# Optimization experiments

Measured on AMD Instinct MI355X. Metric: run time of the kernel, lower is better.

## Reference

```python
import jax, jax.numpy as jnp
import numpy as np

BATCH, K, N, D = 8192, 8, 1024, 256
BETA = 0.25


def setup_inputs() -> dict:
    key = jax.random.key(0)
    kx, ke = jax.random.split(key)
    x = jax.random.normal(kx, (BATCH, K, D), dtype=jnp.float32)
    entries = jax.random.normal(ke, (K, N, D), dtype=jnp.float32)
    return {"x": x, "entries": entries}


def reference(x, entries):
    # x: [b, k, d]; entries: [k, n, d]
    xt = jnp.transpose(x, (1, 0, 2))  # [k, b, d]
    # squared euclidean distances (argmin is identical to cdist argmin)
    d2 = (
        jnp.sum(xt * xt, axis=-1)[:, :, None]
        + jnp.sum(entries * entries, axis=-1)[:, None, :]
        - 2.0 * jnp.einsum("kbd,knd->kbn", xt, entries)
    )  # [k, b, n]
    idx = jnp.argmin(d2, axis=-1)  # [k, b]
    quantized = jnp.take_along_axis(entries, idx[:, :, None], axis=1)  # [k, b, d]
    quantized = jnp.transpose(quantized, (1, 0, 2))  # [b, k, d]
    # straight-through estimator
    x_q = x + jax.lax.stop_gradient(quantized - x)
    dictionary_loss = jnp.mean(
        jnp.sum((jax.lax.stop_gradient(x) - quantized) ** 2, axis=-1)
    )
    commitment_loss = BETA * jnp.mean(
        jnp.sum((x - jax.lax.stop_gradient(quantized)) ** 2, axis=-1)
    )
    return x_q, jnp.transpose(idx, (1, 0)), dictionary_loss, commitment_loss
```

## Files before the change

### kernel.cpp

```cpp
#include <hip/hip_runtime.h>
#include <cstdint>
#include <cstddef>

#define BATCH 8192
#define KC 8
#define NC 1024
#define DC 256
#define TAU 1e-3f

typedef __attribute__((ext_vector_type(8))) _Float16 half8;
typedef __attribute__((ext_vector_type(4))) _Float16 half4;
typedef __attribute__((ext_vector_type(4))) float floatx4;

__device__ __forceinline__ void async_load16(const void* g, void* l) {
    __builtin_amdgcn_global_load_lds((const __attribute__((address_space(1))) uint32_t*)g,
                                     (__attribute__((address_space(3))) uint32_t*)l, 16, 0, 0);
}
__device__ __forceinline__ unsigned sortable(float v) {
    unsigned u = __float_as_uint(v);
    return u ^ (unsigned)(((int)u >> 31) | 0x80000000);
}
__device__ __forceinline__ float unsortable(unsigned ks) {
    unsigned u = (ks & 0x80000000u) ? (ks ^ 0x80000000u) : ~ks;
    return __uint_as_float(u);
}
__device__ __forceinline__ unsigned long long umin64(unsigned long long a, unsigned long long b) { return a < b ? a : b; }
__device__ __forceinline__ unsigned long long umax64(unsigned long long a, unsigned long long b) { return a > b ? a : b; }

__device__ __forceinline__ int lidx(int r, int c) {
    return (r >> 3) * 1024 + (r & 7) * 128 + ((c ^ (r & 7)) * 16);
}
__device__ __forceinline__ half8 ldsr(const char* base, int r, int c) {
    return *(const half8*)(base + lidx(r, c));
}

__global__ __launch_bounds__(256) void prep_e_kernel(const float* __restrict__ entries,
                                                     _Float16* __restrict__ Ecat,
                                                     float* __restrict__ eef) {
    int wave = threadIdx.x >> 6, lane = threadIdx.x & 63;
    int row = blockIdx.x * 4 + wave;
    float4 v = ((const float4*)(entries + (size_t)row * DC))[lane];
    half4 h, l;
    h.x = (_Float16)v.x; h.y = (_Float16)v.y; h.z = (_Float16)v.z; h.w = (_Float16)v.w;
    l.x = (_Float16)(v.x - (float)h.x); l.y = (_Float16)(v.y - (float)h.y);
    l.z = (_Float16)(v.z - (float)h.z); l.w = (_Float16)(v.w - (float)h.w);
    _Float16* rp = Ecat + (size_t)row * 512;
    *(half4*)(rp + lane * 4)       = h;
    *(half4*)(rp + 256 + lane * 4) = l;
    double s = (double)v.x * v.x + (double)v.y * v.y + (double)v.z * v.z + (double)v.w * v.w;
    #pragma unroll
    for (int off = 32; off > 0; off >>= 1) s += __shfl_down(s, off, 64);
    if (lane == 0) eef[row] = (float)s;
}

__global__ __launch_bounds__(256, 2) void vq_gemm(const float* __restrict__ x,
                                                  const float* __restrict__ entries,
                                                  const _Float16* __restrict__ Ecat,
                                                  const float* __restrict__ eef,
                                                  float* __restrict__ out_idx,
                                                  float* __restrict__ out_q,
                                                  double* __restrict__ partial,
                                                  int* __restrict__ flag_list,
                                                  int* __restrict__ flag_cnt) {
    __shared__ alignas(16) char Bh[2][16384];
    __shared__ alignas(16) char Bl[2][16384];
    __shared__ float eef_lds[NC];
    __shared__ unsigned long long top2a[128], top2b[128];
    __shared__ int idx_lds[128];
    __shared__ double red[256];

    const int t = threadIdx.x;
    const int k  = blockIdx.x & 7;
    const int b0 = (blockIdx.x >> 3) * 128;
    const int w = t >> 6, lane = t & 63;
    const int quad = lane >> 4, col = lane & 15;
    const int rl = lane >> 3;
    const int cs = (lane & 7) ^ rl;

    { float4 v = ((const float4*)(eef + (size_t)k * NC))[t]; *(float4*)(eef_lds + t * 4) = v; }
    if (t < 128) { top2a[t] = ~0ull; top2b[t] = ~0ull; }

    half8 Ah[2][8], Al[2][8];
    #pragma unroll
    for (int mi = 0; mi < 2; ++mi) {
        const float* xrow = x + ((size_t)(b0 + w * 32 + mi * 16 + col) * KC + k) * DC + quad * 8;
        #pragma unroll
        for (int ks = 0; ks < 8; ++ks) {
            float4 u0 = *(const float4*)(xrow + ks * 32);
            float4 u1 = *(const float4*)(xrow + ks * 32 + 4);
            float f[8] = {u0.x, u0.y, u0.z, u0.w, u1.x, u1.y, u1.z, u1.w};
            half8 h, l;
            #pragma unroll
            for (int j = 0; j < 8; ++j) {
                h[j] = (_Float16)f[j];
                l[j] = (_Float16)(f[j] - (float)h[j]);
            }
            Ah[mi][ks] = h; Al[mi][ks] = l;
        }
    }

    const char* EcatK = (const char*)(Ecat + (size_t)k * NC * 512);
    #define ISSUE_B(buf, n0b, dcb)                                                          \
        {                                                                                   \
            _Pragma("unroll")                                                               \
            for (int j = 0; j < 8; ++j) {                                                   \
                int li = w * 8 + j; int tile = li >> 4, grp = li & 15;                      \
                const char* src = EcatK + (size_t)((n0b) + grp * 8 + rl) * 1024             \
                                + tile * 512 + (dcb) * 2 + cs * 16;                         \
                char* dst = (tile ? Bl[buf] : Bh[buf]) + grp * 1024 + lane * 16;            \
                async_load16(src, dst);                                                     \
            }                                                                               \
        }

    ISSUE_B(0, 0, 0);

    for (int nt = 0; nt < 8; ++nt) {
        const int n0 = nt * 128;
        floatx4 acc[2][8] = {};
        #pragma unroll
        for (int dcs = 0; dcs < 4; ++dcs) {
            const int step = nt * 4 + dcs;
            __syncthreads();
            if (step < 31) {
                const int ns = step + 1;
                ISSUE_B(ns & 1, (ns >> 2) * 128, (ns & 3) * 64);
            }
            const int cur = step & 1;
            #pragma unroll
            for (int kk = 0; kk < 2; ++kk) {
                const int cb = kk * 4 + quad;
                const int ks = dcs * 2 + kk;
                #pragma unroll
                for (int ni = 0; ni < 8; ++ni) {
                    half8 bh = ldsr(Bh[cur], ni * 16 + col, cb);
                    acc[0][ni] = __builtin_amdgcn_mfma_f32_16x16x32_f16(Ah[0][ks], bh, acc[0][ni], 0, 0, 0);
                    acc[1][ni] = __builtin_amdgcn_mfma_f32_16x16x32_f16(Ah[1][ks], bh, acc[1][ni], 0, 0, 0);
                    acc[0][ni] = __builtin_amdgcn_mfma_f32_16x16x32_f16(Al[0][ks], bh, acc[0][ni], 0, 0, 0);
                    acc[1][ni] = __builtin_amdgcn_mfma_f32_16x16x32_f16(Al[1][ks], bh, acc[1][ni], 0, 0, 0);
                    half8 bl = ldsr(Bl[cur], ni * 16 + col, cb);
                    acc[0][ni] = __builtin_amdgcn_mfma_f32_16x16x32_f16(Ah[0][ks], bl, acc[0][ni], 0, 0, 0);
                    acc[1][ni] = __builtin_amdgcn_mfma_f32_16x16x32_f16(Ah[1][ks], bl, acc[1][ni], 0, 0, 0);
                }
            }
        }
        float ev[8];
        #pragma unroll
        for (int ni = 0; ni < 8; ++ni) ev[ni] = eef_lds[n0 + ni * 16 + col];
        #pragma unroll
        for (int mi = 0; mi < 2; ++mi) {
            #pragma unroll
            for (int reg = 0; reg < 4; ++reg) {
                unsigned long long a1 = ~0ull, a2 = ~0ull;
                #pragma unroll
                for (int ni = 0; ni < 8; ++ni) {
                    float val = fmaf(-2.0f, acc[mi][ni][reg], ev[ni]);
                    unsigned long long key = (((unsigned long long)sortable(val)) << 32)
                                           | (unsigned)(n0 + ni * 16 + col);
                    bool lt1 = key < a1, lt2 = key < a2;
                    a2 = lt1 ? a1 : (lt2 ? key : a2);
                    a1 = lt1 ? key : a1;
                }
                #pragma unroll
                for (int off = 1; off < 16; off <<= 1) {
                    unsigned long long o1 = __shfl_xor(a1, off, 16);
                    unsigned long long o2 = __shfl_xor(a2, off, 16);
                    unsigned long long m1 = umin64(a1, o1);
                    unsigned long long m2 = umin64(umax64(a1, o1), umin64(a2, o2));
                    a1 = m1; a2 = m2;
                }
                if (col == 0) {
                    int row = w * 32 + mi * 16 + quad * 4 + reg;
                    unsigned long long t1 = top2a[row], t2 = top2b[row];
                    top2a[row] = umin64(t1, a1);
                    top2b[row] = umin64(umax64(t1, a1), umin64(t2, a2));
                }
            }
        }
    }

    __syncthreads();
    if (t < 128) {
        unsigned long long a1 = top2a[t], a2 = top2b[t];
        float v1 = unsortable((unsigned)(a1 >> 32));
        float v2 = unsortable((unsigned)(a2 >> 32));
        int rid = (b0 + t) * KC + k;
        if (v2 - v1 < TAU) {
            int pos = atomicAdd(flag_cnt, 1);
            flag_list[pos] = rid;
            idx_lds[t] = -1;
        } else {
            int n = (int)(unsigned)(a1 & 0xFFFFFFFFull);
            idx_lds[t] = n;
            out_idx[rid] = (float)n;
        }
    }
    __syncthreads();

    double s = 0.0;
    #pragma unroll
    for (int rr = 0; rr < 8; ++rr) {
        int r = rr * 16 + (t >> 4);
        int c = t & 15;
        int n = idx_lds[r];
        if (n >= 0) {
            const float4* xp = (const float4*)(x + ((size_t)(b0 + r) * KC + k) * DC);
            const float4* ep = (const float4*)(entries + ((size_t)k * NC + n) * DC);
            float4* op = (float4*)(out_q + ((size_t)(b0 + r) * KC + k) * DC);
            #pragma unroll
            for (int j = 0; j < 4; ++j) {
                int ci = j * 16 + c;
                float4 xv = xp[ci], evv = ep[ci];
                op[ci] = evv;
                double d0 = (double)xv.x - evv.x, d1 = (double)xv.y - evv.y;
                double d2 = (double)xv.z - evv.z, d3 = (double)xv.w - evv.w;
                s += d0 * d0 + d1 * d1 + d2 * d2 + d3 * d3;
            }
        }
    }
    red[t] = s;
    __syncthreads();
    for (int off2 = 128; off2 > 0; off2 >>= 1) {
        if (t < off2) red[t] += red[t + off2];
        __syncthreads();
    }
    if (t == 0) partial[blockIdx.x] = red[0];
    #undef ISSUE_B
}

__global__ __launch_bounds__(256) void refine_kernel(const float* __restrict__ x,
                                                     const float* __restrict__ entries,
                                                     const int* __restrict__ flag_list,
                                                     const int* __restrict__ flag_cnt,
                                                     float* __restrict__ out_idx,
                                                     float* __restrict__ out_q,
                                                     double* __restrict__ refAcc) {
    __shared__ float xs[DC];
    __shared__ double bd[256];
    __shared__ int    bi[256];
    __shared__ int    win;
    const int t = threadIdx.x;
    int cnt = *flag_cnt;
    for (int i = blockIdx.x; i < cnt; i += gridDim.x) {
        int rid = flag_list[i];
        int k = rid & 7;
        __syncthreads();
        xs[t] = x[(size_t)rid * DC + t];
        __syncthreads();
        double best = 1.0e300; int bn = 0;
        for (int e = 0; e < 4; ++e) {
            int n = t * 4 + e;
            const float* ep = entries + ((size_t)k * NC + n) * DC;
            double s = 0.0;
            for (int d = 0; d < DC; ++d) {
                double df = (double)xs[d] - (double)ep[d];
                s += df * df;
            }
            if (s < best) { best = s; bn = n; }
        }
        bd[t] = best; bi[t] = bn;
        __syncthreads();
        for (int s2 = 128; s2 > 0; s2 >>= 1) {
            if (t < s2) {
                if (bd[t + s2] < bd[t] || (bd[t + s2] == bd[t] && bi[t + s2] < bi[t])) {
                    bd[t] = bd[t + s2]; bi[t] = bi[t + s2];
                }
            }
            __syncthreads();
        }
        if (t == 0) {
            out_idx[rid] = (float)bi[0];
            win = bi[0];
            atomicAdd(refAcc, bd[0]);
        }
        __syncthreads();
        out_q[(size_t)rid * DC + t] = entries[((size_t)k * NC + win) * DC + t];
    }
}

__global__ __launch_bounds__(256) void finalize_kernel(const double* __restrict__ partial,
                                                       const double* __restrict__ refAcc,
                                                       float* __restrict__ out) {
    __shared__ double red[256];
    const int t = threadIdx.x;
    double s = 0.0;
    for (int i = t; i < 512; i += 256) s += partial[i];
    red[t] = s;
    __syncthreads();
    for (int off = 128; off > 0; off >>= 1) {
        if (t < off) red[t] += red[t + off];
        __syncthreads();
    }
    if (t == 0) {
        double L = (red[0] + *refAcc) * (1.0 / 65536.0);
        out[(size_t)BATCH * KC * DC + BATCH * KC + 0] = (float)L;
        out[(size_t)BATCH * KC * DC + BATCH * KC + 1] = (float)(0.25 * L);
    }
}

extern "C" void kernel_launch(void* const* d_in, const int* in_sizes, int n_in,
                              void* d_out, int out_size, void* d_ws, size_t ws_size,
                              hipStream_t stream) {
    const float* x       = (const float*)d_in[0];
    const float* entries = (const float*)d_in[1];
    float* out = (float*)d_out;

    char* ws = (char*)d_ws;
    int*      flag_cnt  = (int*)ws;
    double*   refAcc    = (double*)(ws + 8);
    double*   partial   = (double*)(ws + 4096);
    float*    eef       = (float*)(ws + 65536);
    int*      flag_list = (int*)(ws + 131072);
    _Float16* Ecat      = (_Float16*)(ws + 1048576);

    float* out_q   = out;
    float* out_idx = out + (size_t)BATCH * KC * DC;

    hipMemsetAsync(ws, 0, 16, stream);
    prep_e_kernel<<<KC * NC / 4, 256, 0, stream>>>(entries, Ecat, eef);
    vq_gemm<<<512, 256, 0, stream>>>(x, entries, Ecat, eef, out_idx, out_q,
                                     partial, flag_list, flag_cnt);
    refine_kernel<<<128, 256, 0, stream>>>(x, entries, flag_list, flag_cnt,
                                           out_idx, out_q, refAcc);
    finalize_kernel<<<1, 256, 0, stream>>>(partial, refAcc, out);
}
```

Baseline: 274.8 us.

## Use float top-2 argmin tracking and wave-parallel refine distance computation

Replaces the packed 64-bit sortable key top-2 tracking in the GEMM epilogue with separate float values and an int index, cutting 64-bit compares and shuffles in the argmin reduction. Separately, the refine kernel now assigns one codebook entry per wave iteration with lanes splitting the dimension, giving coalesced float4 loads and shuffle reductions. Previously each thread looped serially over 256 dimensions with strided loads. Tie-breaking on equal distances may now favour a different index within the GEMM epilogue, which the refine fallback only partly covers.

After: 372.7 us. +35.6%, slower.

```diff
diff --git a/kernel.cpp b/kernel.cpp
--- a/kernel.cpp
+++ b/kernel.cpp
@@ -16,16 +16,6 @@
     __builtin_amdgcn_global_load_lds((const __attribute__((address_space(1))) uint32_t*)g,
                                      (__attribute__((address_space(3))) uint32_t*)l, 16, 0, 0);
 }
-__device__ __forceinline__ unsigned sortable(float v) {
-    unsigned u = __float_as_uint(v);
-    return u ^ (unsigned)(((int)u >> 31) | 0x80000000);
-}
-__device__ __forceinline__ float unsortable(unsigned ks) {
-    unsigned u = (ks & 0x80000000u) ? (ks ^ 0x80000000u) : ~ks;
-    return __uint_as_float(u);
-}
-__device__ __forceinline__ unsigned long long umin64(unsigned long long a, unsigned long long b) { return a < b ? a : b; }
-__device__ __forceinline__ unsigned long long umax64(unsigned long long a, unsigned long long b) { return a > b ? a : b; }
 
 __device__ __forceinline__ int lidx(int r, int c) {
     return (r >> 3) * 1024 + (r & 7) * 128 + ((c ^ (r & 7)) * 16);
@@ -65,7 +55,9 @@
     __shared__ alignas(16) char Bh[2][16384];
     __shared__ alignas(16) char Bl[2][16384];
     __shared__ float eef_lds[NC];
-    __shared__ unsigned long long top2a[128], top2b[128];
+    __shared__ float tv1[128];
+    __shared__ float tv2[128];
+    __shared__ int   ti1[128];
     __shared__ int idx_lds[128];
     __shared__ double red[256];
 
@@ -78,7 +70,7 @@
     const int cs = (lane & 7) ^ rl;
 
     { float4 v = ((const float4*)(eef + (size_t)k * NC))[t]; *(float4*)(eef_lds + t * 4) = v; }
-    if (t < 128) { top2a[t] = ~0ull; top2b[t] = ~0ull; }
+    if (t < 128) { tv1[t] = 1e30f; tv2[t] = 1e30f; ti1[t] = 0; }
 
     half8 Ah[2][8], Al[2][8];
     #pragma unroll
@@ -150,29 +142,37 @@
         for (int mi = 0; mi < 2; ++mi) {
             #pragma unroll
             for (int reg = 0; reg < 4; ++reg) {
-                unsigned long long a1 = ~0ull, a2 = ~0ull;
+                float v1 = 1e30f, v2 = 1e30f; int i1 = 0;
                 #pragma unroll
                 for (int ni = 0; ni < 8; ++ni) {
                     float val = fmaf(-2.0f, acc[mi][ni][reg], ev[ni]);
-                    unsigned long long key = (((unsigned long long)sortable(val)) << 32)
-                                           | (unsigned)(n0 + ni * 16 + col);
-                    bool lt1 = key < a1, lt2 = key < a2;
-                    a2 = lt1 ? a1 : (lt2 ? key : a2);
-                    a1 = lt1 ? key : a1;
+                    int n = n0 + ni * 16 + col;
+                    bool lt1 = val < v1;
+                    bool lt2 = val < v2;
+                    float nv2 = lt1 ? v1 : (lt2 ? val : v2);
+                    v1 = lt1 ? val : v1;
+                    i1 = lt1 ? n : i1;
+                    v2 = nv2;
                 }
                 #pragma unroll
                 for (int off = 1; off < 16; off <<= 1) {
-                    unsigned long long o1 = __shfl_xor(a1, off, 16);
-                    unsigned long long o2 = __shfl_xor(a2, off, 16);
-                    unsigned long long m1 = umin64(a1, o1);
-                    unsigned long long m2 = umin64(umax64(a1, o1), umin64(a2, o2));
-                    a1 = m1; a2 = m2;
+                    float o1 = __shfl_xor(v1, off, 16);
+                    float o2 = __shfl_xor(v2, off, 16);
+                    int   oi = __shfl_xor(i1, off, 16);
+                    bool sw = o1 < v1;
+                    float hi = sw ? v1 : o1;
+                    v1 = sw ? o1 : v1;
+                    i1 = sw ? oi : i1;
+                    v2 = fminf(fminf(v2, o2), hi);
                 }
                 if (col == 0) {
                     int row = w * 32 + mi * 16 + quad * 4 + reg;
-                    unsigned long long t1 = top2a[row], t2 = top2b[row];
-                    top2a[row] = umin64(t1, a1);
-                    top2b[row] = umin64(umax64(t1, a1), umin64(t2, a2));
+                    float t1 = tv1[row], t2 = tv2[row];
+                    bool sw = v1 < t1;
+                    float hi = sw ? t1 : v1;
+                    tv2[row] = fminf(fminf(t2, v2), hi);
+                    tv1[row] = sw ? v1 : t1;
+                    if (sw) ti1[row] = i1;
                 }
             }
         }
@@ -180,16 +180,14 @@
 
     __syncthreads();
     if (t < 128) {
-        unsigned long long a1 = top2a[t], a2 = top2b[t];
-        float v1 = unsortable((unsigned)(a1 >> 32));
-        float v2 = unsortable((unsigned)(a2 >> 32));
+        float v1 = tv1[t], v2 = tv2[t];
         int rid = (b0 + t) * KC + k;
         if (v2 - v1 < TAU) {
             int pos = atomicAdd(flag_cnt, 1);
             flag_list[pos] = rid;
             idx_lds[t] = -1;
         } else {
-            int n = (int)(unsigned)(a1 & 0xFFFFFFFFull);
+            int n = ti1[t];
             idx_lds[t] = n;
             out_idx[rid] = (float)n;
         }
@@ -234,46 +232,44 @@
                                                      float* __restrict__ out_idx,
                                                      float* __restrict__ out_q,
                                                      double* __restrict__ refAcc) {
-    __shared__ float xs[DC];
-    __shared__ double bd[256];
-    __shared__ int    bi[256];
+    __shared__ double wbest[4];
+    __shared__ int    wbn[4];
     __shared__ int    win;
     const int t = threadIdx.x;
+    const int wave = t >> 6, lane = t & 63;
     int cnt = *flag_cnt;
     for (int i = blockIdx.x; i < cnt; i += gridDim.x) {
         int rid = flag_list[i];
         int k = rid & 7;
-        __syncthreads();
-        xs[t] = x[(size_t)rid * DC + t];
-        __syncthreads();
+        float4 xv = ((const float4*)(x + (size_t)rid * DC))[lane];
+        double x0 = xv.x, x1 = xv.y, x2 = xv.z, x3 = xv.w;
         double best = 1.0e300; int bn = 0;
-        for (int e = 0; e < 4; ++e) {
-            int n = t * 4 + e;
-            const float* ep = entries + ((size_t)k * NC + n) * DC;
-            double s = 0.0;
-            for (int d = 0; d < DC; ++d) {
-                double df = (double)xs[d] - (double)ep[d];
-                s += df * df;
-            }
-            if (s < best) { best = s; bn = n; }
-        }
-        bd[t] = best; bi[t] = bn;
-        __syncthreads();
-        for (int s2 = 128; s2 > 0; s2 >>= 1) {
-            if (t < s2) {
-                if (bd[t + s2] < bd[t] || (bd[t + s2] == bd[t] && bi[t + s2] < bi[t])) {
-                    bd[t] = bd[t + s2]; bi[t] = bi[t + s2];
-                }
-            }
-            __syncthreads();
-        }
+        for (int e = 0; e < 256; ++e) {
+            int n = wave * 256 + e;
+            float4 ev = ((const float4*)(entries + ((size_t)k * NC + n) * DC))[lane];
+            double d0 = x0 - (double)ev.x, d1 = x1 - (double)ev.y;
+            double d2 = x2 - (double)ev.z, d3 = x3 - (double)ev.w;
+            double s = d0 * d0 + d1 * d1 + d2 * d2 + d3 * d3;
+            #pragma unroll
+            for (int off = 32; off > 0; off >>= 1) s += __shfl_down(s, off, 64);
+            if (lane == 0 && s < best) { best = s; bn = n; }
+        }
+        if (lane == 0) { wbest[wave] = best; wbn[wave] = bn; }
+        __syncthreads();
         if (t == 0) {
-            out_idx[rid] = (float)bi[0];
-            win = bi[0];
-            atomicAdd(refAcc, bd[0]);
+            double b = wbest[0]; int n = wbn[0];
+            for (int wv = 1; wv < 4; ++wv) {
+                if (wbest[wv] < b || (wbest[wv] == b && wbn[wv] < n)) {
+                    b = wbest[wv]; n = wbn[wv];
+                }
+            }
+            out_idx[rid] = (float)n;
+            win = n;
+            atomicAdd(refAcc, b);
         }
         __syncthreads();
         out_q[(size_t)rid * DC + t] = entries[((size_t)k * NC + win) * DC + t];
+        __syncthreads();
     }
 }
 
```
